# Kernel tuning notes

Hardware: AMD Instinct MI355X
Metric: run time of the kernel (lower is better)

Reference implementation:

```python
import jax, jax.numpy as jnp
import numpy as np

C64 = jnp.complex64


def _apply_1q(state, G, wire):
    # state: [B,2,2,2,2]; G: [2,2] (shared) or [B,2,2] (per-sample)
    s = jnp.moveaxis(state, wire + 1, -1)
    if G.ndim == 2:
        s = jnp.einsum('ij,b...j->b...i', G, s)
    else:
        s = jnp.einsum('bij,b...j->b...i', G, s)
    return jnp.moveaxis(s, -1, wire + 1)


def _apply_cnot(state, c, t):
    s = jnp.moveaxis(state, (c + 1, t + 1), (-2, -1))
    s = jnp.concatenate([s[..., :1, :], s[..., 1:, ::-1]], axis=-2)
    return jnp.moveaxis(s, (-2, -1), (c + 1, t + 1))


def _rx_batch(theta):
    # theta: [B,4] -> gates [B,4,2,2] (PennyLane AngleEmbedding default = RX)
    c = jnp.cos(theta * 0.5).astype(C64)
    s = (-1j * jnp.sin(theta * 0.5)).astype(C64)
    return jnp.stack([jnp.stack([c, s], -1), jnp.stack([s, c], -1)], -2)


def _ry(theta):
    c = jnp.cos(theta * 0.5).astype(C64)
    s = jnp.sin(theta * 0.5).astype(C64)
    return jnp.stack([jnp.stack([c, -s]), jnp.stack([s, c])])


def _rz(theta):
    t = theta.astype(C64)
    return jnp.diag(jnp.stack([jnp.exp(-0.5j * t), jnp.exp(0.5j * t)]))


def _circuit(features, q_params):
    # features: [B,4] angles, q_params: [8]. Returns <Z_w> per wire: [B,4]
    B = features.shape[0]
    state = jnp.zeros((B, 2, 2, 2, 2), C64).at[:, 0, 0, 0, 0].set(1.0)
    Gx = _rx_batch(features)  # [B,4,2,2]
    for w in range(4):
        state = _apply_1q(state, Gx[:, w], w)
    for w in range(4):
        state = _apply_1q(state, _ry(q_params[w]), w)
    for w in range(3):
        state = _apply_cnot(state, w, w + 1)
    for w in range(4):
        state = _apply_1q(state, _rz(q_params[4 + w]), w)
    probs = state.real ** 2 + state.imag ** 2  # [B,2,2,2,2]
    sign = jnp.array([1.0, -1.0], jnp.float32)
    exps = [jnp.sum(probs * sign.reshape([1] + [2 if a == w else 1 for a in range(4)]),
                    axis=(1, 2, 3, 4)) for w in range(4)]
    return jnp.stack(exps, -1)


def setup_inputs() -> dict:
    key = jax.random.key(0)
    ks = jax.random.split(key, 8)
    B = 65536
    return {
        'x': jax.random.normal(ks[0], (B, 1, 36, 36), jnp.float32),
        'q_params': jax.random.normal(ks[1], (8,), jnp.float32),
        'W1': jax.random.normal(ks[2], (64, 4), jnp.float32) * 0.5,
        'b1': jax.random.normal(ks[3], (64,), jnp.float32) * 0.1,
        'W2': jax.random.normal(ks[4], (4, 64), jnp.float32) * 0.125,
        'b2': jax.random.normal(ks[5], (4,), jnp.float32) * 0.1,
        'gamma': jnp.ones((4,), jnp.float32),
        'beta': jnp.zeros((4,), jnp.float32),
    }


def reference(x, q_params, W1, b1, W2, b2, gamma, beta):
    B = x.shape[0]
    # avg_pool2d(kernel=6, stride=6) on [B,1,36,36] -> [B,1,6,6] -> flatten
    pooled = x.reshape(B, 1, 6, 6, 6, 6).mean(axis=(3, 5)).reshape(B, -1)
    features = pooled[:, :4]
    q_out = _circuit(features, q_params)             # [B,4]
    h = jax.nn.relu(q_out @ W1.T + b1)               # [B,64]
    logits = h @ W2.T + b2                           # [B,4]
    # BatchNorm1d (training mode: batch stats, biased var, eps=1e-5)
    mu = logits.mean(axis=0)
    var = ((logits - mu) ** 2).mean(axis=0)
    return gamma * (logits - mu) / jnp.sqrt(var + 1e-5) + beta
```

## Files before the change

### kernel.cpp

```cpp
#include <hip/hip_runtime.h>
#include <math.h>


__global__ void k_init(float* acc) {
    if (threadIdx.x < 8) acc[threadIdx.x] = 0.0f;
}

#define IMGS_PER_BLOCK 64

__global__ __launch_bounds__(256) void k_main(
    const float* __restrict__ x,
    const float* __restrict__ qp,
    const float* __restrict__ W1,
    const float* __restrict__ b1,
    const float* __restrict__ W2,
    const float* __restrict__ b2,
    float* __restrict__ logits,
    float* __restrict__ acc,
    int B)
{
    __shared__ float sW1[256];
    __shared__ float sW2t[256];
    __shared__ float sb1[64];
    __shared__ float sfeat[IMGS_PER_BLOCK][4];
    __shared__ float sred[32];

    const int tid = threadIdx.x;
    sW1[tid]  = W1[tid];
    sW2t[tid] = W2[(tid & 3) * 64 + (tid >> 2)];
    if (tid < 64) sb1[tid] = b1[tid];

    const int g = tid >> 4, l = tid & 15;
    const int img_base = blockIdx.x * IMGS_PER_BLOCK;

    #pragma unroll
    for (int r = 0; r < 4; ++r) {
        const int li  = r * 16 + g;
        const int img = img_base + li;
        float f0 = 0.f, f1 = 0.f, f2 = 0.f, f3 = 0.f;
        if (img < B) {
            const float* xb = x + (size_t)img * 1296;
            #pragma unroll
            for (int k = 0; k < 3; ++k) {
                const int idx = l + k * 16;
                if (k == 2 && l >= 4) break;
                const int row = (idx * 43) >> 8;
                const int col = idx - 6 * row;
                float4 v = ((const float4*)(xb + row * 36))[col];
                float lo = v.x + v.y, hi = v.z + v.w, tot = lo + hi;
                f0 += (col == 0) ? tot : (col == 1) ? lo : 0.f;
                f1 += (col == 2) ? tot : (col == 1) ? hi : 0.f;
                f2 += (col == 3) ? tot : (col == 4) ? lo : 0.f;
                f3 += (col == 5) ? tot : (col == 4) ? hi : 0.f;
            }
        }
        #pragma unroll
        for (int m = 1; m < 16; m <<= 1) {
            f0 += __shfl_xor(f0, m, 16);
            f1 += __shfl_xor(f1, m, 16);
            f2 += __shfl_xor(f2, m, 16);
            f3 += __shfl_xor(f3, m, 16);
        }
        if (l == 0) {
            sfeat[li][0] = f0; sfeat[li][1] = f1;
            sfeat[li][2] = f2; sfeat[li][3] = f3;
        }
    }
    __syncthreads();

    float l0 = 0.f, l1 = 0.f, l2 = 0.f, l3 = 0.f;
    const int img = img_base + tid;
    if (tid < IMGS_PER_BLOCK && img < B) {
        const float inv36 = 1.0f / 36.0f;
        float z0 = cosf(qp[0]) * cosf(sfeat[tid][0] * inv36);
        float z1 = cosf(qp[1]) * cosf(sfeat[tid][1] * inv36);
        float z2 = cosf(qp[2]) * cosf(sfeat[tid][2] * inv36);
        float z3 = cosf(qp[3]) * cosf(sfeat[tid][3] * inv36);
        float q0 = z0;
        float q1 = q0 * z1;
        float q2 = q1 * z2;
        float q3 = q2 * z3;

        l0 = b2[0]; l1 = b2[1]; l2 = b2[2]; l3 = b2[3];
        #pragma unroll 8
        for (int j = 0; j < 64; ++j) {
            float h = sb1[j];
            h = fmaf(sW1[4*j+0], q0, h);
            h = fmaf(sW1[4*j+1], q1, h);
            h = fmaf(sW1[4*j+2], q2, h);
            h = fmaxf(fmaf(sW1[4*j+3], q3, h), 0.0f);
            l0 = fmaf(sW2t[4*j+0], h, l0);
            l1 = fmaf(sW2t[4*j+1], h, l1);
            l2 = fmaf(sW2t[4*j+2], h, l2);
            l3 = fmaf(sW2t[4*j+3], h, l3);
        }
        ((float4*)logits)[img] = make_float4(l0, l1, l2, l3);
    }

    float v[8] = {l0, l1, l2, l3, l0*l0, l1*l1, l2*l2, l3*l3};
    #pragma unroll
    for (int off = 32; off >= 1; off >>= 1) {
        #pragma unroll
        for (int i = 0; i < 8; ++i) v[i] += __shfl_down(v[i], off);
    }
    const int lane = tid & 63, wv = tid >> 6;
    if (lane == 0) {
        #pragma unroll
        for (int i = 0; i < 8; ++i) sred[wv * 8 + i] = v[i];
    }
    __syncthreads();
    if (tid < 8) {
        float s = sred[tid] + sred[tid + 8] + sred[tid + 16] + sred[tid + 24];
        atomicAdd(&acc[tid], s);
    }
}

__global__ __launch_bounds__(256) void k_norm(
    const float* __restrict__ logits,
    const float* __restrict__ acc,
    const float* __restrict__ gamma,
    const float* __restrict__ beta,
    float* __restrict__ out,
    int B, float invB)
{
    __shared__ float sc[4], sh[4];
    if (threadIdx.x < 4) {
        const int k = threadIdx.x;
        float mu   = acc[k] * invB;
        float var  = acc[4 + k] * invB - mu * mu;
        float rstd = 1.0f / sqrtf(var + 1e-5f);
        float g = gamma[k] * rstd;
        sc[k] = g;
        sh[k] = beta[k] - mu * g;
    }
    __syncthreads();
    const int b = blockIdx.x * 256 + threadIdx.x;
    if (b >= B) return;
    float4 l = ((const float4*)logits)[b];
    float4 o;
    o.x = fmaf(sc[0], l.x, sh[0]);
    o.y = fmaf(sc[1], l.y, sh[1]);
    o.z = fmaf(sc[2], l.z, sh[2]);
    o.w = fmaf(sc[3], l.w, sh[3]);
    ((float4*)out)[b] = o;
}

extern "C" void kernel_launch(void* const* d_in, const int* in_sizes, int n_in,
                              void* d_out, int out_size, void* d_ws, size_t ws_size,
                              hipStream_t stream) {
    const float* x     = (const float*)d_in[0];
    const float* qp    = (const float*)d_in[1];
    const float* W1    = (const float*)d_in[2];
    const float* b1    = (const float*)d_in[3];
    const float* W2    = (const float*)d_in[4];
    const float* b2    = (const float*)d_in[5];
    const float* gamma = (const float*)d_in[6];
    const float* beta  = (const float*)d_in[7];
    float* out = (float*)d_out;

    const int B = in_sizes[0] / 1296;
    float* acc    = (float*)d_ws;
    float* logits = (float*)d_ws + 64;

    const int nb_main = (B + IMGS_PER_BLOCK - 1) / IMGS_PER_BLOCK;
    const int nb_norm = (B + 255) / 256;
    hipLaunchKernelGGL(k_init, dim3(1), dim3(64), 0, stream, acc);
    hipLaunchKernelGGL(k_main, dim3(nb_main), dim3(256), 0, stream,
                       x, qp, W1, b1, W2, b2, logits, acc, B);
    hipLaunchKernelGGL(k_norm, dim3(nb_norm), dim3(256), 0, stream,
                       logits, acc, gamma, beta, out, B, 1.0f / (float)B);
}
```

Measured before the change: 406.8 us.

## Fuse init, main and batchnorm kernels into one cooperative grid-synced kernel

Replaces the three launches (zero the accumulator, main compute, normalization) with a single cooperative kernel. Each block writes its per-block sums to a workspace buffer, waits at a grid-wide sync, then re-reduces all partials itself. It normalizes the logits it still holds in registers and writes the output directly. This drops the logits round trip through global memory, the atomics and two extra launches. In exchange every block must read all partials, and all 1024 blocks must be co-resident (occupancy hint set to 4 blocks per CU) or the cooperative launch fails.

```diff
diff --git a/kernel.cpp b/kernel.cpp
--- a/kernel.cpp
+++ b/kernel.cpp
@@ -1,29 +1,31 @@
 #include <hip/hip_runtime.h>
+#include <hip/hip_cooperative_groups.h>
 #include <math.h>
 
+namespace cg = cooperative_groups;
 
-__global__ void k_init(float* acc) {
-    if (threadIdx.x < 8) acc[threadIdx.x] = 0.0f;
-}
 
 #define IMGS_PER_BLOCK 64
 
-__global__ __launch_bounds__(256) void k_main(
+__global__ __launch_bounds__(256, 4) void k_fused(
     const float* __restrict__ x,
     const float* __restrict__ qp,
     const float* __restrict__ W1,
     const float* __restrict__ b1,
     const float* __restrict__ W2,
     const float* __restrict__ b2,
-    float* __restrict__ logits,
-    float* __restrict__ acc,
-    int B)
+    const float* __restrict__ gamma,
+    const float* __restrict__ beta,
+    float* __restrict__ out,
+    float* __restrict__ part,
+    int B, float invB)
 {
     __shared__ float sW1[256];
     __shared__ float sW2t[256];
     __shared__ float sb1[64];
     __shared__ float sfeat[IMGS_PER_BLOCK][4];
-    __shared__ float sred[32];
+    __shared__ float sred[256];
+    __shared__ float sc[4], sh[4];
 
     const int tid = threadIdx.x;
     sW1[tid]  = W1[tid];
@@ -42,8 +44,8 @@
             const float* xb = x + (size_t)img * 1296;
             #pragma unroll
             for (int k = 0; k < 3; ++k) {
+                if (k == 2 && l >= 4) break;
                 const int idx = l + k * 16;
-                if (k == 2 && l >= 4) break;
                 const int row = (idx * 43) >> 8;
                 const int col = idx - 6 * row;
                 float4 v = ((const float4*)(xb + row * 36))[col];
@@ -70,7 +72,8 @@
 
     float l0 = 0.f, l1 = 0.f, l2 = 0.f, l3 = 0.f;
     const int img = img_base + tid;
-    if (tid < IMGS_PER_BLOCK && img < B) {
+    const bool active = (tid < IMGS_PER_BLOCK) && (img < B);
+    if (active) {
         const float inv36 = 1.0f / 36.0f;
         float z0 = cosf(qp[0]) * cosf(sfeat[tid][0] * inv36);
         float z1 = cosf(qp[1]) * cosf(sfeat[tid][1] * inv36);
@@ -94,7 +97,6 @@
             l2 = fmaf(sW2t[4*j+2], h, l2);
             l3 = fmaf(sW2t[4*j+3], h, l3);
         }
-        ((float4*)logits)[img] = make_float4(l0, l1, l2, l3);
     }
 
     float v[8] = {l0, l1, l2, l3, l0*l0, l1*l1, l2*l2, l3*l3};
@@ -110,39 +112,43 @@
     }
     __syncthreads();
     if (tid < 8) {
-        float s = sred[tid] + sred[tid + 8] + sred[tid + 16] + sred[tid + 24];
-        atomicAdd(&acc[tid], s);
+        part[blockIdx.x * 8 + tid] =
+            sred[tid] + sred[tid + 8] + sred[tid + 16] + sred[tid + 24];
     }
-}
+    __threadfence();
 
-__global__ __launch_bounds__(256) void k_norm(
-    const float* __restrict__ logits,
-    const float* __restrict__ acc,
-    const float* __restrict__ gamma,
-    const float* __restrict__ beta,
-    float* __restrict__ out,
-    int B, float invB)
-{
-    __shared__ float sc[4], sh[4];
-    if (threadIdx.x < 4) {
-        const int k = threadIdx.x;
-        float mu   = acc[k] * invB;
-        float var  = acc[4 + k] * invB - mu * mu;
-        float rstd = 1.0f / sqrtf(var + 1e-5f);
-        float g = gamma[k] * rstd;
-        sc[k] = g;
-        sh[k] = beta[k] - mu * g;
+    cg::this_grid().sync();
+
+    const int total = gridDim.x * 8;
+    float s = 0.f;
+    for (int i = tid; i < total; i += 256) s += part[i];
+    sred[tid] = s;
+    __syncthreads();
+    if (tid < 8) {
+        float t = 0.f;
+        #pragma unroll
+        for (int j = 0; j < 32; ++j) t += sred[tid + 8 * j];
+        sred[tid] = t;
     }
     __syncthreads();
-    const int b = blockIdx.x * 256 + threadIdx.x;
-    if (b >= B) return;
-    float4 l = ((const float4*)logits)[b];
-    float4 o;
-    o.x = fmaf(sc[0], l.x, sh[0]);
-    o.y = fmaf(sc[1], l.y, sh[1]);
-    o.z = fmaf(sc[2], l.z, sh[2]);
-    o.w = fmaf(sc[3], l.w, sh[3]);
-    ((float4*)out)[b] = o;
+    if (tid < 4) {
+        float mu   = sred[tid] * invB;
+        float var  = sred[4 + tid] * invB - mu * mu;
+        float rstd = 1.0f / sqrtf(var + 1e-5f);
+        float gg   = gamma[tid] * rstd;
+        sc[tid] = gg;
+        sh[tid] = beta[tid] - mu * gg;
+    }
+    __syncthreads();
+
+    if (active) {
+        float4 o;
+        o.x = fmaf(sc[0], l0, sh[0]);
+        o.y = fmaf(sc[1], l1, sh[1]);
+        o.z = fmaf(sc[2], l2, sh[2]);
+        o.w = fmaf(sc[3], l3, sh[3]);
+        ((float4*)out)[img] = o;
+    }
 }
 
 extern "C" void kernel_launch(void* const* d_in, const int* in_sizes, int n_in,
@@ -156,17 +162,16 @@
     const float* b2    = (const float*)d_in[5];
     const float* gamma = (const float*)d_in[6];
     const float* beta  = (const float*)d_in[7];
-    float* out = (float*)d_out;
+    float* out  = (float*)d_out;
+    float* part = (float*)d_ws;
 
-    const int B = in_sizes[0] / 1296;
-    float* acc    = (float*)d_ws;
-    float* logits = (float*)d_ws + 64;
+    int B = in_sizes[0] / 1296;
+    float invB = 1.0f / (float)B;
+    int nb = (B + IMGS_PER_BLOCK - 1) / IMGS_PER_BLOCK;
 
-    const int nb_main = (B + IMGS_PER_BLOCK - 1) / IMGS_PER_BLOCK;
-    const int nb_norm = (B + 255) / 256;
-    hipLaunchKernelGGL(k_init, dim3(1), dim3(64), 0, stream, acc);
-    hipLaunchKernelGGL(k_main, dim3(nb_main), dim3(256), 0, stream,
-                       x, qp, W1, b1, W2, b2, logits, acc, B);
-    hipLaunchKernelGGL(k_norm, dim3(nb_norm), dim3(256), 0, stream,
-                       logits, acc, gamma, beta, out, B, 1.0f / (float)B);
+    void* args[] = {(void*)&x, (void*)&qp, (void*)&W1, (void*)&b1, (void*)&W2,
+                    (void*)&b2, (void*)&gamma, (void*)&beta, (void*)&out,
+                    (void*)&part, (void*)&B, (void*)&invB};
+    hipLaunchCooperativeKernel((const void*)k_fused, dim3(nb), dim3(256),
+                               args, 0, stream);
 }
```

After: 523.0 us. 28.6% more time.
